# Optimization experiments

Measured on AMD Instinct MI355X. Metric: run time of the kernel, lower is better.

## Reference

```python
import math
import jax, jax.numpy as jnp
import numpy as np

N_NODES = 100000
N_EDGES = 1600000
N_FEATS = 128
HIDDEN = 64
N_CLASSES = 40
N_LAYERS = 8
ALPHA = 0.1
LAMDA = 0.5


def setup_inputs() -> dict:
    key = jax.random.key(0)
    ks = jax.random.split(key, 6)
    x = jax.random.normal(ks[0], (N_NODES, N_FEATS), dtype=jnp.float32)
    edge_index = jax.random.randint(ks[1], (2, N_EDGES), 0, N_NODES, dtype=jnp.int32)
    W0 = jax.random.normal(ks[2], (N_FEATS, HIDDEN), dtype=jnp.float32) / np.sqrt(N_FEATS)
    b0 = jnp.zeros((HIDDEN,), dtype=jnp.float32)
    Wl = jax.random.normal(ks[3], (N_LAYERS, HIDDEN, HIDDEN), dtype=jnp.float32) / np.sqrt(HIDDEN)
    W_out = jax.random.normal(ks[4], (HIDDEN, N_CLASSES), dtype=jnp.float32) / np.sqrt(HIDDEN)
    b_out = jnp.zeros((N_CLASSES,), dtype=jnp.float32)
    return {"x": x, "edge_index": edge_index, "W0": W0, "b0": b0,
            "Wl": Wl, "W_out": W_out, "b_out": b_out}


def _gcn_norm(edge_index, num_nodes, dtype):
    # PyG gcn_norm: add self-loops (fill 1), sym-normalize D^-1/2 A D^-1/2.
    loops = jnp.arange(num_nodes, dtype=edge_index.dtype)
    row = jnp.concatenate([edge_index[0], loops])  # source
    col = jnp.concatenate([edge_index[1], loops])  # target
    w = jnp.ones(row.shape[0], dtype=dtype)
    deg = jax.ops.segment_sum(w, col, num_segments=num_nodes)
    dinv = jnp.where(deg > 0, jax.lax.rsqrt(deg), 0.0).astype(dtype)
    norm = dinv[row] * w * dinv[col]
    return row, col, norm


def _propagate(x, row, col, norm, num_nodes):
    # SpMM: out[i] = sum_{e: col[e]==i} norm[e] * x[row[e]]
    msgs = x[row] * norm[:, None]  # [E+N, H]
    return jax.ops.segment_sum(msgs, col, num_segments=num_nodes)


def reference(x, edge_index, W0, b0, Wl, W_out, b_out):
    n = x.shape[0]
    row, col, norm = _gcn_norm(edge_index, n, x.dtype)
    # eval mode: dropout is identity; non-arxiv dataset: no batchnorm
    h = jax.nn.relu(x @ W0 + b0)
    h0 = h
    for i in range(N_LAYERS):
        agg = _propagate(h, row, col, norm, n)
        support = (1.0 - ALPHA) * agg + ALPHA * h0
        beta = math.log(LAMDA / (i + 1) + 1.0)
        h = jax.nn.relu(beta * (support @ Wl[i]) + (1.0 - beta) * support)
    return h @ W_out + b_out
```

## Files before the change

kernel.cpp:

```cpp
#include <hip/hip_runtime.h>
#include <cmath>

#define N_NODES   100000
#define N_EDGES   1600000
#define N_FEATS   128
#define HIDDEN    64
#define N_CLASSES 40
#define N_LAYERS  8
#define ALPHA     0.1f
#define LAMDA     0.5f

#define SCAN_ITEMS 8
#define SCAN_BLK   256
#define SCAN_TILE  (SCAN_ITEMS * SCAN_BLK)
#define SCAN_NBLK  ((N_NODES + SCAN_TILE - 1) / SCAN_TILE)

#define FILL_RANGES 8
#define RANGE_SIZE  ((N_NODES + FILL_RANGES - 1) / FILL_RANGES)
#define FILL_BLOCKS 1024

typedef unsigned short ushortT;
typedef unsigned int   uintT;

__device__ __forceinline__ float bf2f(ushortT u) {
    return __uint_as_float(((uintT)u) << 16);
}
__device__ __forceinline__ ushortT f2bf(float f) {
    uintT x = __float_as_uint(f);
    return (ushortT)((x + 0x7FFFu + ((x >> 16) & 1u)) >> 16);
}


__global__ __launch_bounds__(256) void k_zero_deg(int* __restrict__ deg) {
    int i = blockIdx.x * 256 + threadIdx.x;
    if (i < N_NODES) deg[i] = 0;
}

__global__ __launch_bounds__(256) void k_count_deg(const int* __restrict__ col,
                                                   int* __restrict__ deg) {
    const int G = gridDim.x * 256;
    int e0 = blockIdx.x * 256 + threadIdx.x;
    int e1 = e0 + G, e2 = e1 + G, e3 = e2 + G;
    int c0 = (e0 < N_EDGES) ? col[e0] : -1;
    int c1 = (e1 < N_EDGES) ? col[e1] : -1;
    int c2 = (e2 < N_EDGES) ? col[e2] : -1;
    int c3 = (e3 < N_EDGES) ? col[e3] : -1;
    if (c0 >= 0) atomicAdd(&deg[c0], 1);
    if (c1 >= 0) atomicAdd(&deg[c1], 1);
    if (c2 >= 0) atomicAdd(&deg[c2], 1);
    if (c3 >= 0) atomicAdd(&deg[c3], 1);
}

__global__ __launch_bounds__(SCAN_BLK) void k_scan1(const int* __restrict__ deg,
                                                    int* __restrict__ rowptr,
                                                    int* __restrict__ bsum) {
    __shared__ int sc[SCAN_BLK];
    const int t = threadIdx.x;
    const int base = blockIdx.x * SCAN_TILE + t * SCAN_ITEMS;
    int v[SCAN_ITEMS];
    int tsum = 0;
#pragma unroll
    for (int j = 0; j < SCAN_ITEMS; ++j) {
        v[j] = (base + j < N_NODES) ? deg[base + j] : 0;
        tsum += v[j];
    }
    sc[t] = tsum;
    __syncthreads();
    for (int off = 1; off < SCAN_BLK; off <<= 1) {
        int x = (t >= off) ? sc[t - off] : 0;
        __syncthreads();
        sc[t] += x;
        __syncthreads();
    }
    int run = sc[t] - tsum;
#pragma unroll
    for (int j = 0; j < SCAN_ITEMS; ++j) {
        if (base + j < N_NODES) rowptr[base + j] = run;
        run += v[j];
    }
    if (t == SCAN_BLK - 1) bsum[blockIdx.x] = sc[SCAN_BLK - 1];
}

__global__ __launch_bounds__(SCAN_BLK) void k_scan2(int* __restrict__ bsum) {
    __shared__ int sc[SCAN_BLK];
    const int t = threadIdx.x;
    int v = (t < SCAN_NBLK) ? bsum[t] : 0;
    sc[t] = v;
    __syncthreads();
    for (int off = 1; off < SCAN_BLK; off <<= 1) {
        int x = (t >= off) ? sc[t - off] : 0;
        __syncthreads();
        sc[t] += x;
        __syncthreads();
    }
    if (t < SCAN_NBLK) bsum[t] = sc[t] - v;
}

__global__ __launch_bounds__(256) void k_scan3(int* __restrict__ rowptr,
                                               const int* __restrict__ bsum,
                                               int* __restrict__ cursor) {
    int i = blockIdx.x * 256 + threadIdx.x;
    if (i < N_NODES) {
        int r = rowptr[i] + bsum[i / SCAN_TILE];
        rowptr[i] = r;
        cursor[i] = r;
    }
    if (i == 0) rowptr[N_NODES] = N_EDGES;
}

__global__ __launch_bounds__(256) void k_dinv(const int* __restrict__ deg,
                                              float* __restrict__ dinv) {
    int i = blockIdx.x * 256 + threadIdx.x;
    if (i < N_NODES) dinv[i] = rsqrtf(1.0f + (float)deg[i]);
}

__global__ __launch_bounds__(256) void k_fill(const int* __restrict__ row,
                                              const int* __restrict__ col,
                                              const float* __restrict__ dinv,
                                              int* __restrict__ cursor,
                                              int2* __restrict__ csr) {
    const int range = blockIdx.x & (FILL_RANGES - 1);
    const int lo = range * RANGE_SIZE;
    const int hi = lo + RANGE_SIZE;
    const int stride = (gridDim.x >> 3) * 256;
    for (int e = (blockIdx.x >> 3) * 256 + threadIdx.x; e < N_EDGES; e += stride) {
        int c = col[e];
        if (c >= lo && c < hi) {
            int r = row[e];
            int pos = atomicAdd(&cursor[c], 1);
            csr[pos] = make_int2(r, __float_as_int((1.0f - ALPHA) * dinv[r] * dinv[c]));
        }
    }
}


__global__ __launch_bounds__(256) void k_gemm_in(const float* __restrict__ x,
                                                 const float* __restrict__ W0,
                                                 const float* __restrict__ b0,
                                                 ushortT* __restrict__ h_bf,
                                                 ushortT* __restrict__ h0_bf) {
    __shared__ float sW[N_FEATS * HIDDEN];
    __shared__ float sX[64 * N_FEATS];
    const int v0 = blockIdx.x * 64;
    const bool full = (v0 + 64 <= N_NODES);

    const float4* W4 = (const float4*)W0;
    for (int idx = threadIdx.x; idx < (N_FEATS * HIDDEN) / 4; idx += 256)
        ((float4*)sW)[idx] = W4[idx];
    if (full) {
        const float4* X4 = (const float4*)(x + (size_t)v0 * N_FEATS);
        for (int idx = threadIdx.x; idx < (64 * N_FEATS) / 4; idx += 256)
            ((float4*)sX)[idx] = X4[idx];
    } else {
        for (int idx = threadIdx.x; idx < 64 * N_FEATS; idx += 256) {
            int r = idx >> 7, k = idx & 127;
            int v = v0 + r;
            sX[idx] = (v < N_NODES) ? x[(size_t)v * N_FEATS + k] : 0.0f;
        }
    }
    __syncthreads();

    const int c  = threadIdx.x & 63;
    const int r0 = threadIdx.x >> 6;
    float acc[16];
#pragma unroll
    for (int j = 0; j < 16; ++j) acc[j] = 0.0f;

    for (int k = 0; k < N_FEATS; ++k) {
        float w = sW[k * HIDDEN + c];
#pragma unroll
        for (int j = 0; j < 16; ++j)
            acc[j] += sX[(r0 + 4 * j) * N_FEATS + k] * w;
    }

    const float bias = b0[c];
#pragma unroll
    for (int j = 0; j < 16; ++j) {
        int v = v0 + r0 + 4 * j;
        if (v < N_NODES) {
            ushortT val = f2bf(fmaxf(acc[j] + bias, 0.0f));
            h_bf [(size_t)v * HIDDEN + c] = val;
            h0_bf[(size_t)v * HIDDEN + c] = val;
        }
    }
}


__global__ __launch_bounds__(256) void k_spmm(const int* __restrict__ rowptr,
                                              const int2* __restrict__ csr,
                                              const float* __restrict__ dinv,
                                              const ushortT* __restrict__ h_bf,
                                              const ushortT* __restrict__ h0_bf,
                                              ushortT* __restrict__ buf_bf) {
    const int lane = threadIdx.x & 63;
    const int l32  = lane & 31;
    const int half = lane >> 5;
    const int node = (blockIdx.x * 256 + threadIdx.x) >> 6;
    if (node >= N_NODES) return;

    const int e0 = rowptr[node];
    const int e1 = rowptr[node + 1];
    const float d = dinv[node];

    float ax, ay;
    if (half == 0) {
        const ushort2 hv  = *(const ushort2*)(h_bf  + (size_t)node * HIDDEN + 2 * l32);
        const ushort2 h0v = *(const ushort2*)(h0_bf + (size_t)node * HIDDEN + 2 * l32);
        const float cs = (1.0f - ALPHA) * d * d;
        ax = cs * bf2f(hv.x) + ALPHA * bf2f(h0v.x);
        ay = cs * bf2f(hv.y) + ALPHA * bf2f(h0v.y);
    } else {
        ax = 0.0f; ay = 0.0f;
    }

    for (int eb = e0; eb < e1; eb += 64) {
        int n = e1 - eb;
        if (n > 64) n = 64;
        int   idx = 0;
        float w   = 0.0f;
        if (lane < n) {
            int2 e = csr[eb + lane];
            idx = e.x;
            w   = __int_as_float(e.y);
        }
        for (int j = 0; j < n; j += 16) {
            int    s[8];
            float  ww[8];
            ushort2 xv[8];
#pragma unroll
            for (int u = 0; u < 8; ++u) {
                int src = j + 2 * u + half;
                s[u]  = __shfl(idx, src);
                ww[u] = __shfl(w, src);
            }
#pragma unroll
            for (int u = 0; u < 8; ++u)
                xv[u] = *(const ushort2*)(h_bf + (size_t)s[u] * HIDDEN + 2 * l32);
#pragma unroll
            for (int u = 0; u < 8; ++u) {
                ax += ww[u] * bf2f(xv[u].x);
                ay += ww[u] * bf2f(xv[u].y);
            }
        }
    }

    ax += __shfl_xor(ax, 32);
    ay += __shfl_xor(ay, 32);
    if (half == 0) {
        ushort2 o; o.x = f2bf(ax); o.y = f2bf(ay);
        *(ushort2*)(buf_bf + (size_t)node * HIDDEN + 2 * l32) = o;
    }
}


__global__ __launch_bounds__(256) void k_gemm_layer(const ushortT* __restrict__ S_bf,
                                                    const float* __restrict__ W,
                                                    float beta,
                                                    ushortT* __restrict__ hout_bf) {
    __shared__ float sW[HIDDEN * HIDDEN];
    __shared__ float sS[64 * HIDDEN];
    const int v0 = blockIdx.x * 64;
    const bool full = (v0 + 64 <= N_NODES);

    const float4* W4 = (const float4*)W;
    for (int idx = threadIdx.x; idx < (HIDDEN * HIDDEN) / 4; idx += 256)
        ((float4*)sW)[idx] = W4[idx];
    if (full) {
        const ushort4* S4 = (const ushort4*)(S_bf + (size_t)v0 * HIDDEN);
        for (int idx = threadIdx.x; idx < (64 * HIDDEN) / 4; idx += 256) {
            ushort4 u = S4[idx];
            sS[idx * 4 + 0] = bf2f(u.x);
            sS[idx * 4 + 1] = bf2f(u.y);
            sS[idx * 4 + 2] = bf2f(u.z);
            sS[idx * 4 + 3] = bf2f(u.w);
        }
    } else {
        for (int idx = threadIdx.x; idx < 64 * HIDDEN; idx += 256) {
            int r = idx >> 6, k = idx & 63;
            int v = v0 + r;
            sS[idx] = (v < N_NODES) ? bf2f(S_bf[(size_t)v * HIDDEN + k]) : 0.0f;
        }
    }
    __syncthreads();

    const int c  = threadIdx.x & 63;
    const int r0 = threadIdx.x >> 6;
    float acc[16];
#pragma unroll
    for (int j = 0; j < 16; ++j) acc[j] = 0.0f;

    for (int k = 0; k < HIDDEN; ++k) {
        float w = sW[k * HIDDEN + c];
#pragma unroll
        for (int j = 0; j < 16; ++j)
            acc[j] += sS[(r0 + 4 * j) * HIDDEN + k] * w;
    }

#pragma unroll
    for (int j = 0; j < 16; ++j) {
        int r = r0 + 4 * j;
        int v = v0 + r;
        if (v < N_NODES) {
            float s   = sS[r * HIDDEN + c];
            float val = fmaxf(beta * acc[j] + (1.0f - beta) * s, 0.0f);
            hout_bf[(size_t)v * HIDDEN + c] = f2bf(val);
        }
    }
}


__global__ __launch_bounds__(256) void k_gemm_out(const ushortT* __restrict__ h_bf,
                                                  const float* __restrict__ Wout,
                                                  const float* __restrict__ bout,
                                                  float* __restrict__ out) {
    __shared__ float sW[HIDDEN * N_CLASSES];
    __shared__ float sH[64 * HIDDEN];
    const int v0 = blockIdx.x * 64;
    const bool full = (v0 + 64 <= N_NODES);

    for (int idx = threadIdx.x; idx < HIDDEN * N_CLASSES; idx += 256)
        sW[idx] = Wout[idx];
    if (full) {
        const ushort4* H4 = (const ushort4*)(h_bf + (size_t)v0 * HIDDEN);
        for (int idx = threadIdx.x; idx < (64 * HIDDEN) / 4; idx += 256) {
            ushort4 u = H4[idx];
            sH[idx * 4 + 0] = bf2f(u.x);
            sH[idx * 4 + 1] = bf2f(u.y);
            sH[idx * 4 + 2] = bf2f(u.z);
            sH[idx * 4 + 3] = bf2f(u.w);
        }
    } else {
        for (int idx = threadIdx.x; idx < 64 * HIDDEN; idx += 256) {
            int r = idx >> 6, k = idx & 63;
            int v = v0 + r;
            sH[idx] = (v < N_NODES) ? bf2f(h_bf[(size_t)v * HIDDEN + k]) : 0.0f;
        }
    }
    __syncthreads();

    for (int idx = threadIdx.x; idx < 64 * N_CLASSES; idx += 256) {
        int r = idx / N_CLASSES, c = idx % N_CLASSES;
        int v = v0 + r;
        if (v < N_NODES) {
            float acc = bout[c];
#pragma unroll 8
            for (int k = 0; k < HIDDEN; ++k)
                acc += sH[r * HIDDEN + k] * sW[k * N_CLASSES + c];
            out[(size_t)v * N_CLASSES + c] = acc;
        }
    }
}


extern "C" void kernel_launch(void* const* d_in, const int* in_sizes, int n_in,
                              void* d_out, int out_size, void* d_ws, size_t ws_size,
                              hipStream_t stream) {
    const float* x    = (const float*)d_in[0];
    const int*   ei   = (const int*)d_in[1];
    const float* W0   = (const float*)d_in[2];
    const float* b0   = (const float*)d_in[3];
    const float* Wl   = (const float*)d_in[4];
    const float* Wout = (const float*)d_in[5];
    const float* bout = (const float*)d_in[6];
    float* out = (float*)d_out;

    const int* row = ei;
    const int* col = ei + N_EDGES;

    char* ws = (char*)d_ws;
    size_t off = 0;
    auto alloc = [&](size_t bytes) -> void* {
        void* p = ws + off;
        off += (bytes + 255) & ~(size_t)255;
        return p;
    };
    int*     deg    = (int*)alloc((size_t)N_NODES * 4);
    int*     rowptr = (int*)alloc((size_t)(N_NODES + 1) * 4);
    int*     cursor = (int*)alloc((size_t)N_NODES * 4);
    int*     bsum   = (int*)alloc((size_t)SCAN_NBLK * 4);
    int2*    csr    = (int2*)alloc((size_t)N_EDGES * 8);
    float*   dinv   = (float*)alloc((size_t)N_NODES * 4);
    ushortT* h0_bf  = (ushortT*)alloc((size_t)N_NODES * HIDDEN * 2);
    ushortT* buf_bf = (ushortT*)alloc((size_t)N_NODES * HIDDEN * 2);
    ushortT* h_bf   = (ushortT*)alloc((size_t)N_NODES * HIDDEN * 2);

    const int gN   = (N_NODES + 255) / 256;
    const int gRow = (N_NODES + 63) / 64;
    const int gSpm = (N_NODES * 64 + 255) / 256;
    const int gE4  = (N_EDGES + 4 * 256 - 1) / (4 * 256);

    k_zero_deg <<<gN, 256, 0, stream>>>(deg);
    k_count_deg<<<gE4, 256, 0, stream>>>(col, deg);
    k_scan1    <<<SCAN_NBLK, SCAN_BLK, 0, stream>>>(deg, rowptr, bsum);
    k_scan2    <<<1, SCAN_BLK, 0, stream>>>(bsum);
    k_scan3    <<<gN, 256, 0, stream>>>(rowptr, bsum, cursor);
    k_dinv     <<<gN, 256, 0, stream>>>(deg, dinv);
    k_fill     <<<FILL_BLOCKS, 256, 0, stream>>>(row, col, dinv, cursor, csr);

    k_gemm_in<<<gRow, 256, 0, stream>>>(x, W0, b0, h_bf, h0_bf);

    for (int i = 0; i < N_LAYERS; ++i) {
        float beta = logf(LAMDA / (float)(i + 1) + 1.0f);
        k_spmm<<<gSpm, 256, 0, stream>>>(rowptr, csr, dinv, h_bf, h0_bf, buf_bf);
        k_gemm_layer<<<gRow, 256, 0, stream>>>(buf_bf, Wl + (size_t)i * HIDDEN * HIDDEN,
                                               beta, h_bf);
    }

    k_gemm_out<<<gRow, 256, 0, stream>>>(h_bf, Wout, bout, out);
}
```

Before: 798.0 us.

## Store hidden features in 16-feature chunked layout and split SpMM by chunk

Hidden activations are now stored as four feature chunks of 16 bf16 values per node (chunk-major), and the SpMM grid is split by chunk so each wave gathers 32-byte rows from one 3.2 MB chunk. The aim is to make the random neighbor gathers hit in cache, since each chunk's working set is far smaller than the full feature matrix. In exchange each wave handles 8 edges at once with 8 lanes per edge, uses more shuffle reductions, and rereads the CSR edge list once per chunk. The GEMM kernels are adapted to read and write the chunked layout.

```diff
diff --git a/kernel.cpp b/kernel.cpp
--- a/kernel.cpp
+++ b/kernel.cpp
@@ -19,6 +19,10 @@
 #define RANGE_SIZE  ((N_NODES + FILL_RANGES - 1) / FILL_RANGES)
 #define FILL_BLOCKS 1024
 
+#define CHUNKS 4
+#define CF     16
+#define SPMM_BPC ((N_NODES + 3) / 4)
+
 typedef unsigned short ushortT;
 typedef unsigned int   uintT;
 
@@ -28,6 +32,9 @@
 __device__ __forceinline__ ushortT f2bf(float f) {
     uintT x = __float_as_uint(f);
     return (ushortT)((x + 0x7FFFu + ((x >> 16) & 1u)) >> 16);
+}
+__device__ __forceinline__ size_t chunked_off(int v, int c) {
+    return ((size_t)(c >> 4) * N_NODES + v) * CF + (c & 15);
 }
 
 
@@ -179,8 +186,9 @@
         int v = v0 + r0 + 4 * j;
         if (v < N_NODES) {
             ushortT val = f2bf(fmaxf(acc[j] + bias, 0.0f));
-            h_bf [(size_t)v * HIDDEN + c] = val;
-            h0_bf[(size_t)v * HIDDEN + c] = val;
+            size_t o = chunked_off(v, c);
+            h_bf [o] = val;
+            h0_bf[o] = val;
         }
     }
 }
@@ -192,26 +200,20 @@
                                               const ushortT* __restrict__ h_bf,
                                               const ushortT* __restrict__ h0_bf,
                                               ushortT* __restrict__ buf_bf) {
+    const int wv   = threadIdx.x >> 6;
     const int lane = threadIdx.x & 63;
-    const int l32  = lane & 31;
-    const int half = lane >> 5;
-    const int node = (blockIdx.x * 256 + threadIdx.x) >> 6;
+    const int g    = lane >> 3;
+    const int fl   = lane & 7;
+    const int chunk = blockIdx.x / SPMM_BPC;
+    const int node  = (blockIdx.x % SPMM_BPC) * 4 + wv;
     if (node >= N_NODES) return;
+
+    const ushortT* hC = h_bf + (size_t)chunk * N_NODES * CF;
 
     const int e0 = rowptr[node];
     const int e1 = rowptr[node + 1];
-    const float d = dinv[node];
-
-    float ax, ay;
-    if (half == 0) {
-        const ushort2 hv  = *(const ushort2*)(h_bf  + (size_t)node * HIDDEN + 2 * l32);
-        const ushort2 h0v = *(const ushort2*)(h0_bf + (size_t)node * HIDDEN + 2 * l32);
-        const float cs = (1.0f - ALPHA) * d * d;
-        ax = cs * bf2f(hv.x) + ALPHA * bf2f(h0v.x);
-        ay = cs * bf2f(hv.y) + ALPHA * bf2f(h0v.y);
-    } else {
-        ax = 0.0f; ay = 0.0f;
-    }
+
+    float ax = 0.0f, ay = 0.0f;
 
     for (int eb = e0; eb < e1; eb += 64) {
         int n = e1 - eb;
@@ -224,31 +226,33 @@
             w   = __int_as_float(e.y);
         }
         for (int j = 0; j < n; j += 16) {
-            int    s[8];
-            float  ww[8];
-            ushort2 xv[8];
-#pragma unroll
-            for (int u = 0; u < 8; ++u) {
-                int src = j + 2 * u + half;
-                s[u]  = __shfl(idx, src);
-                ww[u] = __shfl(w, src);
-            }
-#pragma unroll
-            for (int u = 0; u < 8; ++u)
-                xv[u] = *(const ushort2*)(h_bf + (size_t)s[u] * HIDDEN + 2 * l32);
-#pragma unroll
-            for (int u = 0; u < 8; ++u) {
-                ax += ww[u] * bf2f(xv[u].x);
-                ay += ww[u] * bf2f(xv[u].y);
-            }
-        }
-    }
-
-    ax += __shfl_xor(ax, 32);
-    ay += __shfl_xor(ay, 32);
-    if (half == 0) {
-        ushort2 o; o.x = f2bf(ax); o.y = f2bf(ay);
-        *(ushort2*)(buf_bf + (size_t)node * HIDDEN + 2 * l32) = o;
+            int   s0 = __shfl(idx, j + g);
+            int   s1 = __shfl(idx, j + 8 + g);
+            float w0 = __shfl(w, j + g);
+            float w1 = __shfl(w, j + 8 + g);
+            uintT v0 = *(const uintT*)(hC + (size_t)s0 * CF + 2 * fl);
+            uintT v1 = *(const uintT*)(hC + (size_t)s1 * CF + 2 * fl);
+            ax += w0 * bf2f((ushortT)(v0 & 0xFFFFu));
+            ay += w0 * bf2f((ushortT)(v0 >> 16));
+            ax += w1 * bf2f((ushortT)(v1 & 0xFFFFu));
+            ay += w1 * bf2f((ushortT)(v1 >> 16));
+        }
+    }
+
+    ax += __shfl_xor(ax, 8);  ay += __shfl_xor(ay, 8);
+    ax += __shfl_xor(ax, 16); ay += __shfl_xor(ay, 16);
+    ax += __shfl_xor(ax, 32); ay += __shfl_xor(ay, 32);
+
+    if (g == 0) {
+        const float d  = dinv[node];
+        const float cs = (1.0f - ALPHA) * d * d;
+        const size_t so = (size_t)chunk * N_NODES * CF + (size_t)node * CF + 2 * fl;
+        uintT hv  = *(const uintT*)(h_bf  + so);
+        uintT h0v = *(const uintT*)(h0_bf + so);
+        float rx = cs * bf2f((ushortT)(hv & 0xFFFFu)) + ALPHA * bf2f((ushortT)(h0v & 0xFFFFu)) + ax;
+        float ry = cs * bf2f((ushortT)(hv >> 16))     + ALPHA * bf2f((ushortT)(h0v >> 16))     + ay;
+        ushort2 o; o.x = f2bf(rx); o.y = f2bf(ry);
+        *(ushort2*)(buf_bf + so) = o;
     }
 }
 
@@ -266,19 +270,23 @@
     for (int idx = threadIdx.x; idx < (HIDDEN * HIDDEN) / 4; idx += 256)
         ((float4*)sW)[idx] = W4[idx];
     if (full) {
-        const ushort4* S4 = (const ushort4*)(S_bf + (size_t)v0 * HIDDEN);
-        for (int idx = threadIdx.x; idx < (64 * HIDDEN) / 4; idx += 256) {
-            ushort4 u = S4[idx];
-            sS[idx * 4 + 0] = bf2f(u.x);
-            sS[idx * 4 + 1] = bf2f(u.y);
-            sS[idx * 4 + 2] = bf2f(u.z);
-            sS[idx * 4 + 3] = bf2f(u.w);
+        for (int idx = threadIdx.x; idx < 1024; idx += 256) {
+            int chunk = idx >> 8;
+            int rem   = idx & 255;
+            int r     = rem >> 2;
+            int slot  = rem & 3;
+            ushort4 u = ((const ushort4*)(S_bf + ((size_t)chunk * N_NODES + v0 + r) * CF))[slot];
+            int f = chunk * 16 + slot * 4;
+            sS[r * HIDDEN + f + 0] = bf2f(u.x);
+            sS[r * HIDDEN + f + 1] = bf2f(u.y);
+            sS[r * HIDDEN + f + 2] = bf2f(u.z);
+            sS[r * HIDDEN + f + 3] = bf2f(u.w);
         }
     } else {
         for (int idx = threadIdx.x; idx < 64 * HIDDEN; idx += 256) {
             int r = idx >> 6, k = idx & 63;
             int v = v0 + r;
-            sS[idx] = (v < N_NODES) ? bf2f(S_bf[(size_t)v * HIDDEN + k]) : 0.0f;
+            sS[idx] = (v < N_NODES) ? bf2f(S_bf[chunked_off(v, k)]) : 0.0f;
         }
     }
     __syncthreads();
@@ -303,7 +311,7 @@
         if (v < N_NODES) {
             float s   = sS[r * HIDDEN + c];
             float val = fmaxf(beta * acc[j] + (1.0f - beta) * s, 0.0f);
-            hout_bf[(size_t)v * HIDDEN + c] = f2bf(val);
+            hout_bf[chunked_off(v, c)] = f2bf(val);
         }
     }
 }
@@ -321,19 +329,23 @@
     for (int idx = threadIdx.x; idx < HIDDEN * N_CLASSES; idx += 256)
         sW[idx] = Wout[idx];
     if (full) {
-        const ushort4* H4 = (const ushort4*)(h_bf + (size_t)v0 * HIDDEN);
-        for (int idx = threadIdx.x; idx < (64 * HIDDEN) / 4; idx += 256) {
-            ushort4 u = H4[idx];
-            sH[idx * 4 + 0] = bf2f(u.x);
-            sH[idx * 4 + 1] = bf2f(u.y);
-            sH[idx * 4 + 2] = bf2f(u.z);
-            sH[idx * 4 + 3] = bf2f(u.w);
+        for (int idx = threadIdx.x; idx < 1024; idx += 256) {
+            int chunk = idx >> 8;
+            int rem   = idx & 255;
+            int r     = rem >> 2;
+            int slot  = rem & 3;
+            ushort4 u = ((const ushort4*)(h_bf + ((size_t)chunk * N_NODES + v0 + r) * CF))[slot];
+            int f = chunk * 16 + slot * 4;
+            sH[r * HIDDEN + f + 0] = bf2f(u.x);
+            sH[r * HIDDEN + f + 1] = bf2f(u.y);
+            sH[r * HIDDEN + f + 2] = bf2f(u.z);
+            sH[r * HIDDEN + f + 3] = bf2f(u.w);
         }
     } else {
         for (int idx = threadIdx.x; idx < 64 * HIDDEN; idx += 256) {
             int r = idx >> 6, k = idx & 63;
             int v = v0 + r;
-            sH[idx] = (v < N_NODES) ? bf2f(h_bf[(size_t)v * HIDDEN + k]) : 0.0f;
+            sH[idx] = (v < N_NODES) ? bf2f(h_bf[chunked_off(v, k)]) : 0.0f;
         }
     }
     __syncthreads();
@@ -386,7 +398,7 @@
 
     const int gN   = (N_NODES + 255) / 256;
     const int gRow = (N_NODES + 63) / 64;
-    const int gSpm = (N_NODES * 64 + 255) / 256;
+    const int gSpm = CHUNKS * SPMM_BPC;
     const int gE4  = (N_EDGES + 4 * 256 - 1) / (4 * 256);
 
     k_zero_deg <<<gN, 256, 0, stream>>>(deg);
```

Result: slower. 1.399 ms (+75.3%).

## Split SpMM into four source-range passes for gather cache locality

Applied to the files above, without the earlier changes.

Edges are bucketed by both source-node range (four ranges) and destination, so the CSR is ordered by (source range, target). Each layer now runs four SpMM passes, each gathering only from a quarter of h, so the gathered rows (about 3.2MB per pass) fit better in L2/MALL. Partial sums accumulate into a new fp32 intermediate buffer that is read and rewritten on every pass. The cost is four times the launches and rowptr reads, plus extra fp32 read-modify-write traffic on the accumulator, and the degree, scan and cursor arrays become four times larger.

```diff
diff --git a/kernel.cpp b/kernel.cpp
--- a/kernel.cpp
+++ b/kernel.cpp
@@ -10,10 +10,14 @@
 #define ALPHA     0.1f
 #define LAMDA     0.5f
 
+#define SR_CNT   4
+#define SR_SIZE  ((N_NODES + SR_CNT - 1) / SR_CNT)
+#define NBUCKET  (SR_CNT * N_NODES)
+
 #define SCAN_ITEMS 8
 #define SCAN_BLK   256
 #define SCAN_TILE  (SCAN_ITEMS * SCAN_BLK)
-#define SCAN_NBLK  ((N_NODES + SCAN_TILE - 1) / SCAN_TILE)
+#define SCAN_NBLK  ((NBUCKET + SCAN_TILE - 1) / SCAN_TILE)
 
 #define FILL_RANGES 8
 #define RANGE_SIZE  ((N_NODES + FILL_RANGES - 1) / FILL_RANGES)
@@ -31,28 +35,30 @@
 }
 
 
-__global__ __launch_bounds__(256) void k_zero_deg(int* __restrict__ deg) {
+__global__ __launch_bounds__(256) void k_zero_deg(int* __restrict__ deg4) {
     int i = blockIdx.x * 256 + threadIdx.x;
-    if (i < N_NODES) deg[i] = 0;
-}
-
-__global__ __launch_bounds__(256) void k_count_deg(const int* __restrict__ col,
-                                                   int* __restrict__ deg) {
+    if (i < NBUCKET) deg4[i] = 0;
+}
+
+__global__ __launch_bounds__(256) void k_count_deg(const int* __restrict__ row,
+                                                   const int* __restrict__ col,
+                                                   int* __restrict__ deg4) {
     const int G = gridDim.x * 256;
     int e0 = blockIdx.x * 256 + threadIdx.x;
     int e1 = e0 + G, e2 = e1 + G, e3 = e2 + G;
-    int c0 = (e0 < N_EDGES) ? col[e0] : -1;
-    int c1 = (e1 < N_EDGES) ? col[e1] : -1;
-    int c2 = (e2 < N_EDGES) ? col[e2] : -1;
-    int c3 = (e3 < N_EDGES) ? col[e3] : -1;
-    if (c0 >= 0) atomicAdd(&deg[c0], 1);
-    if (c1 >= 0) atomicAdd(&deg[c1], 1);
-    if (c2 >= 0) atomicAdd(&deg[c2], 1);
-    if (c3 >= 0) atomicAdd(&deg[c3], 1);
-}
-
-__global__ __launch_bounds__(SCAN_BLK) void k_scan1(const int* __restrict__ deg,
-                                                    int* __restrict__ rowptr,
+    int b0 = -1, b1 = -1, b2 = -1, b3 = -1;
+    if (e0 < N_EDGES) b0 = (row[e0] / SR_SIZE) * N_NODES + col[e0];
+    if (e1 < N_EDGES) b1 = (row[e1] / SR_SIZE) * N_NODES + col[e1];
+    if (e2 < N_EDGES) b2 = (row[e2] / SR_SIZE) * N_NODES + col[e2];
+    if (e3 < N_EDGES) b3 = (row[e3] / SR_SIZE) * N_NODES + col[e3];
+    if (b0 >= 0) atomicAdd(&deg4[b0], 1);
+    if (b1 >= 0) atomicAdd(&deg4[b1], 1);
+    if (b2 >= 0) atomicAdd(&deg4[b2], 1);
+    if (b3 >= 0) atomicAdd(&deg4[b3], 1);
+}
+
+__global__ __launch_bounds__(SCAN_BLK) void k_scan1(const int* __restrict__ deg4,
+                                                    int* __restrict__ rowptr4,
                                                     int* __restrict__ bsum) {
     __shared__ int sc[SCAN_BLK];
     const int t = threadIdx.x;
@@ -61,7 +67,7 @@
     int tsum = 0;
 #pragma unroll
     for (int j = 0; j < SCAN_ITEMS; ++j) {
-        v[j] = (base + j < N_NODES) ? deg[base + j] : 0;
+        v[j] = (base + j < NBUCKET) ? deg4[base + j] : 0;
         tsum += v[j];
     }
     sc[t] = tsum;
@@ -75,7 +81,7 @@
     int run = sc[t] - tsum;
 #pragma unroll
     for (int j = 0; j < SCAN_ITEMS; ++j) {
-        if (base + j < N_NODES) rowptr[base + j] = run;
+        if (base + j < NBUCKET) rowptr4[base + j] = run;
         run += v[j];
     }
     if (t == SCAN_BLK - 1) bsum[blockIdx.x] = sc[SCAN_BLK - 1];
@@ -96,28 +102,31 @@
     if (t < SCAN_NBLK) bsum[t] = sc[t] - v;
 }
 
-__global__ __launch_bounds__(256) void k_scan3(int* __restrict__ rowptr,
+__global__ __launch_bounds__(256) void k_scan3(int* __restrict__ rowptr4,
                                                const int* __restrict__ bsum,
-                                               int* __restrict__ cursor) {
+                                               int* __restrict__ cursor4) {
+    int i = blockIdx.x * 256 + threadIdx.x;
+    if (i < NBUCKET) {
+        int r = rowptr4[i] + bsum[i / SCAN_TILE];
+        rowptr4[i] = r;
+        cursor4[i] = r;
+    }
+    if (i == 0) rowptr4[NBUCKET] = N_EDGES;
+}
+
+__global__ __launch_bounds__(256) void k_dinv(const int* __restrict__ deg4,
+                                              float* __restrict__ dinv) {
     int i = blockIdx.x * 256 + threadIdx.x;
     if (i < N_NODES) {
-        int r = rowptr[i] + bsum[i / SCAN_TILE];
-        rowptr[i] = r;
-        cursor[i] = r;
-    }
-    if (i == 0) rowptr[N_NODES] = N_EDGES;
-}
-
-__global__ __launch_bounds__(256) void k_dinv(const int* __restrict__ deg,
-                                              float* __restrict__ dinv) {
-    int i = blockIdx.x * 256 + threadIdx.x;
-    if (i < N_NODES) dinv[i] = rsqrtf(1.0f + (float)deg[i]);
+        int d = deg4[i] + deg4[N_NODES + i] + deg4[2 * N_NODES + i] + deg4[3 * N_NODES + i];
+        dinv[i] = rsqrtf(1.0f + (float)d);
+    }
 }
 
 __global__ __launch_bounds__(256) void k_fill(const int* __restrict__ row,
                                               const int* __restrict__ col,
                                               const float* __restrict__ dinv,
-                                              int* __restrict__ cursor,
+                                              int* __restrict__ cursor4,
                                               int2* __restrict__ csr) {
     const int range = blockIdx.x & (FILL_RANGES - 1);
     const int lo = range * RANGE_SIZE;
@@ -127,7 +136,7 @@
         int c = col[e];
         if (c >= lo && c < hi) {
             int r = row[e];
-            int pos = atomicAdd(&cursor[c], 1);
+            int pos = atomicAdd(&cursor4[(r / SR_SIZE) * N_NODES + c], 1);
             csr[pos] = make_int2(r, __float_as_int((1.0f - ALPHA) * dinv[r] * dinv[c]));
         }
     }
@@ -186,32 +195,23 @@
 }
 
 
-__global__ __launch_bounds__(256) void k_spmm(const int* __restrict__ rowptr,
+__global__ __launch_bounds__(256) void k_spmm(int pass,
+                                              const int* __restrict__ rowptr4,
                                               const int2* __restrict__ csr,
                                               const float* __restrict__ dinv,
                                               const ushortT* __restrict__ h_bf,
                                               const ushortT* __restrict__ h0_bf,
-                                              ushortT* __restrict__ buf_bf) {
+                                              float* __restrict__ buf) {
     const int lane = threadIdx.x & 63;
     const int l32  = lane & 31;
     const int half = lane >> 5;
     const int node = (blockIdx.x * 256 + threadIdx.x) >> 6;
     if (node >= N_NODES) return;
 
-    const int e0 = rowptr[node];
-    const int e1 = rowptr[node + 1];
-    const float d = dinv[node];
-
-    float ax, ay;
-    if (half == 0) {
-        const ushort2 hv  = *(const ushort2*)(h_bf  + (size_t)node * HIDDEN + 2 * l32);
-        const ushort2 h0v = *(const ushort2*)(h0_bf + (size_t)node * HIDDEN + 2 * l32);
-        const float cs = (1.0f - ALPHA) * d * d;
-        ax = cs * bf2f(hv.x) + ALPHA * bf2f(h0v.x);
-        ay = cs * bf2f(hv.y) + ALPHA * bf2f(h0v.y);
-    } else {
-        ax = 0.0f; ay = 0.0f;
-    }
+    const int e0 = rowptr4[pass * N_NODES + node];
+    const int e1 = rowptr4[pass * N_NODES + node + 1];
+
+    float ax = 0.0f, ay = 0.0f;
 
     for (int eb = e0; eb < e1; eb += 64) {
         int n = e1 - eb;
@@ -246,14 +246,29 @@
 
     ax += __shfl_xor(ax, 32);
     ay += __shfl_xor(ay, 32);
+
     if (half == 0) {
-        ushort2 o; o.x = f2bf(ax); o.y = f2bf(ay);
-        *(ushort2*)(buf_bf + (size_t)node * HIDDEN + 2 * l32) = o;
-    }
-}
-
-
-__global__ __launch_bounds__(256) void k_gemm_layer(const ushortT* __restrict__ S_bf,
+        float2* bp = (float2*)(buf + (size_t)node * HIDDEN + 2 * l32);
+        if (pass == 0) {
+            const float d  = dinv[node];
+            const float cs = (1.0f - ALPHA) * d * d;
+            const ushort2 hv  = *(const ushort2*)(h_bf  + (size_t)node * HIDDEN + 2 * l32);
+            const ushort2 h0v = *(const ushort2*)(h0_bf + (size_t)node * HIDDEN + 2 * l32);
+            float2 o;
+            o.x = cs * bf2f(hv.x) + ALPHA * bf2f(h0v.x) + ax;
+            o.y = cs * bf2f(hv.y) + ALPHA * bf2f(h0v.y) + ay;
+            *bp = o;
+        } else {
+            float2 o = *bp;
+            o.x += ax;
+            o.y += ay;
+            *bp = o;
+        }
+    }
+}
+
+
+__global__ __launch_bounds__(256) void k_gemm_layer(const float* __restrict__ S,
                                                     const float* __restrict__ W,
                                                     float beta,
                                                     ushortT* __restrict__ hout_bf) {
@@ -266,19 +281,14 @@
     for (int idx = threadIdx.x; idx < (HIDDEN * HIDDEN) / 4; idx += 256)
         ((float4*)sW)[idx] = W4[idx];
     if (full) {
-        const ushort4* S4 = (const ushort4*)(S_bf + (size_t)v0 * HIDDEN);
-        for (int idx = threadIdx.x; idx < (64 * HIDDEN) / 4; idx += 256) {
-            ushort4 u = S4[idx];
-            sS[idx * 4 + 0] = bf2f(u.x);
-            sS[idx * 4 + 1] = bf2f(u.y);
-            sS[idx * 4 + 2] = bf2f(u.z);
-            sS[idx * 4 + 3] = bf2f(u.w);
-        }
+        const float4* S4 = (const float4*)(S + (size_t)v0 * HIDDEN);
+        for (int idx = threadIdx.x; idx < (64 * HIDDEN) / 4; idx += 256)
+            ((float4*)sS)[idx] = S4[idx];
     } else {
         for (int idx = threadIdx.x; idx < 64 * HIDDEN; idx += 256) {
             int r = idx >> 6, k = idx & 63;
             int v = v0 + r;
-            sS[idx] = (v < N_NODES) ? bf2f(S_bf[(size_t)v * HIDDEN + k]) : 0.0f;
+            sS[idx] = (v < N_NODES) ? S[(size_t)v * HIDDEN + k] : 0.0f;
         }
     }
     __syncthreads();
@@ -374,35 +384,37 @@
         off += (bytes + 255) & ~(size_t)255;
         return p;
     };
-    int*     deg    = (int*)alloc((size_t)N_NODES * 4);
-    int*     rowptr = (int*)alloc((size_t)(N_NODES + 1) * 4);
-    int*     cursor = (int*)alloc((size_t)N_NODES * 4);
-    int*     bsum   = (int*)alloc((size_t)SCAN_NBLK * 4);
-    int2*    csr    = (int2*)alloc((size_t)N_EDGES * 8);
-    float*   dinv   = (float*)alloc((size_t)N_NODES * 4);
-    ushortT* h0_bf  = (ushortT*)alloc((size_t)N_NODES * HIDDEN * 2);
-    ushortT* buf_bf = (ushortT*)alloc((size_t)N_NODES * HIDDEN * 2);
-    ushortT* h_bf   = (ushortT*)alloc((size_t)N_NODES * HIDDEN * 2);
-
+    int*     deg4    = (int*)alloc((size_t)NBUCKET * 4);
+    int*     rowptr4 = (int*)alloc((size_t)(NBUCKET + 1) * 4);
+    int*     cursor4 = (int*)alloc((size_t)NBUCKET * 4);
+    int*     bsum    = (int*)alloc((size_t)SCAN_NBLK * 4);
+    int2*    csr     = (int2*)alloc((size_t)N_EDGES * 8);
+    float*   dinv    = (float*)alloc((size_t)N_NODES * 4);
+    ushortT* h0_bf   = (ushortT*)alloc((size_t)N_NODES * HIDDEN * 2);
+    float*   buf     = (float*)alloc((size_t)N_NODES * HIDDEN * 4);
+    ushortT* h_bf    = (ushortT*)alloc((size_t)N_NODES * HIDDEN * 2);
+
+    const int gB   = (NBUCKET + 255) / 256;
     const int gN   = (N_NODES + 255) / 256;
     const int gRow = (N_NODES + 63) / 64;
     const int gSpm = (N_NODES * 64 + 255) / 256;
     const int gE4  = (N_EDGES + 4 * 256 - 1) / (4 * 256);
 
-    k_zero_deg <<<gN, 256, 0, stream>>>(deg);
-    k_count_deg<<<gE4, 256, 0, stream>>>(col, deg);
-    k_scan1    <<<SCAN_NBLK, SCAN_BLK, 0, stream>>>(deg, rowptr, bsum);
+    k_zero_deg <<<gB, 256, 0, stream>>>(deg4);
+    k_count_deg<<<gE4, 256, 0, stream>>>(row, col, deg4);
+    k_scan1    <<<SCAN_NBLK, SCAN_BLK, 0, stream>>>(deg4, rowptr4, bsum);
     k_scan2    <<<1, SCAN_BLK, 0, stream>>>(bsum);
-    k_scan3    <<<gN, 256, 0, stream>>>(rowptr, bsum, cursor);
-    k_dinv     <<<gN, 256, 0, stream>>>(deg, dinv);
-    k_fill     <<<FILL_BLOCKS, 256, 0, stream>>>(row, col, dinv, cursor, csr);
+    k_scan3    <<<gB, 256, 0, stream>>>(rowptr4, bsum, cursor4);
+    k_dinv     <<<gN, 256, 0, stream>>>(deg4, dinv);
+    k_fill     <<<FILL_BLOCKS, 256, 0, stream>>>(row, col, dinv, cursor4, csr);
 
     k_gemm_in<<<gRow, 256, 0, stream>>>(x, W0, b0, h_bf, h0_bf);
 
     for (int i = 0; i < N_LAYERS; ++i) {
         float beta = logf(LAMDA / (float)(i + 1) + 1.0f);
-        k_spmm<<<gSpm, 256, 0, stream>>>(rowptr, csr, dinv, h_bf, h0_bf, buf_bf);
-        k_gemm_layer<<<gRow, 256, 0, stream>>>(buf_bf, Wl + (size_t)i * HIDDEN * HIDDEN,
+        for (int p = 0; p < SR_CNT; ++p)
+            k_spmm<<<gSpm, 256, 0, stream>>>(p, rowptr4, csr, dinv, h_bf, h0_bf, buf);
+        k_gemm_layer<<<gRow, 256, 0, stream>>>(buf, Wl + (size_t)i * HIDDEN * HIDDEN,
                                                beta, h_bf);
     }
 
```

New measurement: 1.425 ms. +78.5%, slower.
